# Kernel tuning notes

Hardware: AMD Instinct MI355X
Metric: run time of the kernel (lower is better)

The kernel has to match this reference:

```python
import jax, jax.numpy as jnp
import numpy as np
import math

N_SCALES = 8
WAVELET_LEN = 64
MIN_SCALE, MAX_SCALE = 1.0, 64.0
BATCH, SEQ, FEAT = 16, 4096, 64


def _morlet_init():
    # Faithful to _initialize_mother_wavelets
    t = np.linspace(-4.0, 4.0, WAVELET_LEN, dtype=np.float32)
    w = np.zeros((N_SCALES, WAVELET_LEN), dtype=np.float32)
    for i in range(N_SCALES):
        omega = 2.0 + i * 0.5
        sigma = 1.0 + i * 0.1
        wav = np.exp(-t ** 2 / (2 * sigma ** 2)) * np.cos(omega * t)
        w[i] = wav / np.linalg.norm(wav)
    return jnp.asarray(w)


def setup_inputs() -> dict:
    key = jax.random.key(0)
    k1, _ = jax.random.split(key)
    signal = jax.random.normal(k1, (BATCH, SEQ, FEAT), dtype=jnp.float32)
    mother_wavelets = _morlet_init()
    scale_weights = jnp.ones((N_SCALES,), dtype=jnp.float32)
    return {"signal": signal, "mother_wavelets": mother_wavelets, "scale_weights": scale_weights}


def _scales():
    return np.logspace(math.log10(MIN_SCALE), math.log10(MAX_SCALE), N_SCALES)


def _dilate(wavelet, scale):
    # F.interpolate(mode='linear', align_corners=True) to length int(WAVELET_LEN*scale)
    L_out = int(WAVELET_LEN * scale)
    if L_out > 1:
        pos = jnp.arange(L_out, dtype=jnp.float32) * ((WAVELET_LEN - 1) / (L_out - 1))
    else:
        pos = jnp.zeros((1,), dtype=jnp.float32)
    grid = jnp.arange(WAVELET_LEN, dtype=jnp.float32)
    return jnp.interp(pos, grid, wavelet) / math.sqrt(scale)


def reference(signal, mother_wavelets, scale_weights):
    # signal: (B, S, F) -> coefficients: (B, n_scales, S, F)
    B, S, F = signal.shape
    sig = jnp.swapaxes(signal, 1, 2)  # (B, F, S): batch all FFTs over b,f per scale
    scales = _scales()
    coeffs = []
    for i in range(N_SCALES):
        s = float(scales[i])
        w = _dilate(mother_wavelets[i], s)  # (L_dil,)
        n = S + w.shape[0] - 1
        n_fft = 2 ** int(math.ceil(math.log2(n)))
        Sf = jnp.fft.rfft(sig, n=n_fft, axis=-1)
        Wf = jnp.fft.rfft(w, n=n_fft)
        conv = jnp.fft.irfft(Sf * Wf, n=n_fft, axis=-1)[..., :S]  # (B, F, S)
        coeffs.append(conv)
    C = jnp.stack(coeffs, axis=1)            # (B, n_scales, F, S)
    C = jnp.swapaxes(C, 2, 3)                # (B, n_scales, S, F)
    return C * scale_weights[None, :, None, None]
```

## Files before the change

### kernel.cpp

```cpp
#include <hip/hip_runtime.h>
#include <hip/hip_bf16.h>
#include <math.h>

typedef __attribute__((ext_vector_type(8))) short bf16x8;
typedef __attribute__((ext_vector_type(4))) float f32x4;
typedef __attribute__((ext_vector_type(4))) unsigned int u32x4;
typedef __attribute__((ext_vector_type(2))) unsigned int u32x2;

#define NSC    8
#define SLEN   4096
#define FEAT   64
#define CHUNK_B 8192

#define W4 10176
#define WG_ELEMS 40960
constexpr int L_[NSC]     = {64, 115, 210, 380, 689, 1248, 2261, 4096};
constexpr int LF_[NSC]    = {132, 196, 292, 452, 772, 1316, 2340, 4164};
constexpr int OFF_[NSC]   = {0, 196, 456, 812, 1328, 2164, 3544, 5948};
constexpr int BASES_[NSC] = {132, 392, 748, 1264, 2100, 3480, 5884, 10112};
constexpr int CACT_[NSC]  = {3, 5, 8, 13, 23, 40, 72, 129};

struct WavP { float step[NSC]; float isq[NSC]; };

__global__ void k_build_wav(const float* __restrict__ mw, const float* __restrict__ sw,
                            __hip_bfloat16* __restrict__ wg, WavP wp)
{
  int e = blockIdx.x * 256 + threadIdx.x;
  if (e >= WG_ELEMS) return;
  float val = 0.f;
  if (e < 4 * W4) {
    int q = e / W4;
    int x = e - q * W4;
    int s = 0;
    #pragma unroll
    for (int i = 1; i < NSC; ++i) if (x >= OFF_[i]) s = i;
    int xl = x - OFF_[s] + q;
    int k = LF_[s] - xl;
    if (k >= 0 && k < L_[s]) {
      float pos = (float)k * wp.step[s];
      int ii = (int)pos;
      float r;
      if (ii >= 63) r = mw[s * 64 + 63];
      else {
        float a = mw[s * 64 + ii];
        r = fmaf(pos - (float)ii, mw[s * 64 + ii + 1] - a, a);
      }
      val = r * wp.isq[s] * sw[s];
    }
  }
  wg[e] = __float2bfloat16(val);
}

__global__ __launch_bounds__(256) void k_transpose(const float* __restrict__ sig,
                                                   __hip_bfloat16* __restrict__ sigT2)
{
  __shared__ float t[4096];
  const int tid = threadIdx.x;
  const float* sp = sig + (size_t)blockIdx.x * 4096;
  for (int idx = tid; idx < 4096; idx += 256) {
    int r = idx >> 6, f = idx & 63;
    t[(r << 6) + (f ^ ((r & 7) << 3))] = sp[idx];
  }
  __syncthreads();
  __hip_bfloat16* op = sigT2 + (size_t)blockIdx.x * 4096;
  for (int e = tid; e < 4096; e += 256) {
    int h = e >> 11, n = (e >> 9) & 3, l = (e >> 3) & 63, i = e & 7;
    int f = n * 16 + (l & 15);
    int r = h * 32 + (l >> 4) * 8 + i;
    op[e] = __float2bfloat16(t[(r << 6) + (f ^ ((r & 7) << 3))]);
  }
}

__global__ __launch_bounds__(256, 2) void k_wavelet_mfma(
    const __hip_bfloat16* __restrict__ sigT2,
    const __hip_bfloat16* __restrict__ wavg,
    float* __restrict__ out)
{
  __shared__ __align__(16) short ldsW[WG_ELEMS];

  const int tid = threadIdx.x;
  const int bid = blockIdx.x;
  const int tt  = 63 - (bid >> 4);
  const int b   = bid & 15;
  const int t0  = tt * 64;
  const int tw  = tid >> 6;
  const int fl  = tid & 15;
  const int g   = (tid >> 4) & 3;

  {
    const char* gp = (const char*)wavg;
    char* lp = (char*)ldsW;
    #pragma unroll
    for (int it = 0; it < 20; ++it)
      __builtin_amdgcn_global_load_lds(
        (const __attribute__((address_space(1))) void*)(gp + it * 4096 + tid * 16),
        (__attribute__((address_space(3))) void*)(lp + it * 4096 + (tid >> 6) * 1024),
        16, 0, 0);
  }
  __syncthreads();

  const int q4    = (16 - fl) & 3;
  const int laneA = q4 * W4 + (32 - 16 * tw + 8 * g - fl - q4);

  const int C = tt + 1;
  const char* cb = (const char*)sigT2 + ((size_t)(b * 64 + tt)) * CHUNK_B
                   + (size_t)(tid & 63) * 16;

  f32x4 acc[NSC][4];
  const f32x4 z = {0.f, 0.f, 0.f, 0.f};
  #pragma unroll
  for (int s = 0; s < NSC; ++s)
    #pragma unroll
    for (int n = 0; n < 4; ++n) acc[s][n] = z;

  bf16x8 Ba[8], Bb[8];
  auto loadchunk = [&](int c, bf16x8* B) {
    const char* p = cb - (size_t)c * CHUNK_B;
    #pragma unroll
    for (int hn = 0; hn < 8; ++hn)
      B[hn] = *(const bf16x8*)(p + (hn >> 2) * 4096 + (hn & 3) * 1024);
  };

  auto compute = [&](int c_old, const bf16x8* Bf) {
    const int abase = laneA - 32 * c_old;
    __builtin_amdgcn_s_setprio(1);
    #pragma unroll
    for (int s = NSC - 1; s >= 0; --s) {
      if (c_old <= CACT_[s]) {
        const u32x2* pp = (const u32x2*)(ldsW + abase + BASES_[s]);
        u32x2 w0 = pp[0], w1 = pp[1];
        u32x4 au; au.x = w0.x; au.y = w0.y; au.z = w1.x; au.w = w1.y;
        bf16x8 Af = __builtin_bit_cast(bf16x8, au);
        acc[s][0] = __builtin_amdgcn_mfma_f32_16x16x32_bf16(Af, Bf[0], acc[s][0], 0, 0, 0);
        acc[s][1] = __builtin_amdgcn_mfma_f32_16x16x32_bf16(Af, Bf[1], acc[s][1], 0, 0, 0);
        acc[s][2] = __builtin_amdgcn_mfma_f32_16x16x32_bf16(Af, Bf[2], acc[s][2], 0, 0, 0);
        acc[s][3] = __builtin_amdgcn_mfma_f32_16x16x32_bf16(Af, Bf[3], acc[s][3], 0, 0, 0);
      }
    }
    __builtin_amdgcn_s_setprio(0);
  };

  loadchunk(0, Ba);

  for (int c = 0; c < C; c += 2) {
    loadchunk(c + 1, Bb);
    compute(2 * c,     &Ba[4]);
    compute(2 * c + 1, &Ba[0]);
    loadchunk(c + 2, Ba);
    if (c + 1 < C) {
      compute(2 * c + 2, &Bb[4]);
      compute(2 * c + 3, &Bb[0]);
    }
  }

  const int trow = t0 + tw * 16 + g * 4;
  float* ob = out + (size_t)b * NSC * SLEN * FEAT;
  #pragma unroll
  for (int s = 0; s < NSC; ++s) {
    float* os = ob + (size_t)s * SLEN * FEAT;
    #pragma unroll
    for (int n = 0; n < 4; ++n)
      #pragma unroll
      for (int r = 0; r < 4; ++r)
        os[(size_t)(trow + r) * FEAT + n * 16 + fl] = acc[s][n][r];
  }
}

extern "C" void kernel_launch(void* const* d_in, const int* in_sizes, int n_in,
                              void* d_out, int out_size, void* d_ws, size_t ws_size,
                              hipStream_t stream) {
  const float* sig = (const float*)d_in[0];
  const float* mw  = (const float*)d_in[1];
  const float* sw  = (const float*)d_in[2];
  float*       out = (float*)d_out;

  __hip_bfloat16* wavg  = (__hip_bfloat16*)d_ws;
  __hip_bfloat16* sigT2 = (__hip_bfloat16*)((char*)d_ws + 131072);

  WavP wp;
  const double lg = log10(64.0), st = lg / 7.0;
  for (int i = 0; i < NSC; ++i) {
    double y = (i == 7) ? lg : (double)i * st;
    double s = pow(10.0, y);
    int L = L_[i];
    wp.step[i] = (float)(63.0 / (double)(L - 1));
    wp.isq[i]  = (float)(1.0 / sqrt(s));
  }

  k_build_wav<<<WG_ELEMS / 256, 256, 0, stream>>>(mw, sw, wavg, wp);
  k_transpose<<<1024, 256, 0, stream>>>(sig, sigT2);
  k_wavelet_mfma<<<1024, 256, 0, stream>>>(sigT2, wavg, out);
}
```

Baseline: 83.66 us.

## Replace LDS wavelet staging with precomputed per-lane A-fragment table in global memory

Builds a fully expanded table of bf16 A fragments (one 16-byte vector per lane per scale per quarter-chunk) in global memory, so the main kernel loads A operands directly with vector global loads. This removes the 80KB LDS staging, the block-wide barrier and the unaligned two-part LDS reads. The B-chunk double buffer is also restructured into half-chunk granularity. The cost is about 2MB of table traffic served from L2 instead of LDS, plus extra global load latency inside the MFMA loop.

```diff
diff --git a/kernel.cpp b/kernel.cpp
--- a/kernel.cpp
+++ b/kernel.cpp
@@ -4,51 +4,38 @@
 
 typedef __attribute__((ext_vector_type(8))) short bf16x8;
 typedef __attribute__((ext_vector_type(4))) float f32x4;
-typedef __attribute__((ext_vector_type(4))) unsigned int u32x4;
-typedef __attribute__((ext_vector_type(2))) unsigned int u32x2;
 
 #define NSC    8
 #define SLEN   4096
 #define FEAT   64
 #define CHUNK_B 8192
+#define NQ     258
+#define ATAB_B (NQ * 8 * 1024)
 
-#define W4 10176
-#define WG_ELEMS 40960
-constexpr int L_[NSC]     = {64, 115, 210, 380, 689, 1248, 2261, 4096};
-constexpr int LF_[NSC]    = {132, 196, 292, 452, 772, 1316, 2340, 4164};
-constexpr int OFF_[NSC]   = {0, 196, 456, 812, 1328, 2164, 3544, 5948};
-constexpr int BASES_[NSC] = {132, 392, 748, 1264, 2100, 3480, 5884, 10112};
-constexpr int CACT_[NSC]  = {3, 5, 8, 13, 23, 40, 72, 129};
+constexpr int L_[NSC]    = {64, 115, 210, 380, 689, 1248, 2261, 4096};
+constexpr int CACT_[NSC] = {3, 5, 8, 13, 23, 40, 72, 129};
 
 struct WavP { float step[NSC]; float isq[NSC]; };
 
-__global__ void k_build_wav(const float* __restrict__ mw, const float* __restrict__ sw,
-                            __hip_bfloat16* __restrict__ wg, WavP wp)
+__global__ void k_build_atab(const float* __restrict__ mw, const float* __restrict__ sw,
+                             __hip_bfloat16* __restrict__ at, WavP wp)
 {
   int e = blockIdx.x * 256 + threadIdx.x;
-  if (e >= WG_ELEMS) return;
+  int j = e & 7, l = (e >> 3) & 63, s = (e >> 9) & 7, q = e >> 12;
+  int k = 16 * q - 32 + (l & 15) - 8 * (l >> 4) - j;
   float val = 0.f;
-  if (e < 4 * W4) {
-    int q = e / W4;
-    int x = e - q * W4;
-    int s = 0;
-    #pragma unroll
-    for (int i = 1; i < NSC; ++i) if (x >= OFF_[i]) s = i;
-    int xl = x - OFF_[s] + q;
-    int k = LF_[s] - xl;
-    if (k >= 0 && k < L_[s]) {
-      float pos = (float)k * wp.step[s];
-      int ii = (int)pos;
-      float r;
-      if (ii >= 63) r = mw[s * 64 + 63];
-      else {
-        float a = mw[s * 64 + ii];
-        r = fmaf(pos - (float)ii, mw[s * 64 + ii + 1] - a, a);
-      }
-      val = r * wp.isq[s] * sw[s];
+  if (k >= 0 && k < L_[s]) {
+    float pos = (float)k * wp.step[s];
+    int ii = (int)pos;
+    float r;
+    if (ii >= 63) r = mw[s * 64 + 63];
+    else {
+      float a = mw[s * 64 + ii];
+      r = fmaf(pos - (float)ii, mw[s * 64 + ii + 1] - a, a);
     }
+    val = r * wp.isq[s] * sw[s];
   }
-  wg[e] = __float2bfloat16(val);
+  at[e] = __float2bfloat16(val);
 }
 
 __global__ __launch_bounds__(256) void k_transpose(const float* __restrict__ sig,
@@ -73,38 +60,23 @@
 
 __global__ __launch_bounds__(256, 2) void k_wavelet_mfma(
     const __hip_bfloat16* __restrict__ sigT2,
-    const __hip_bfloat16* __restrict__ wavg,
+    const __hip_bfloat16* __restrict__ atab,
     float* __restrict__ out)
 {
-  __shared__ __align__(16) short ldsW[WG_ELEMS];
-
   const int tid = threadIdx.x;
   const int bid = blockIdx.x;
   const int tt  = 63 - (bid >> 4);
   const int b   = bid & 15;
   const int t0  = tt * 64;
   const int tw  = tid >> 6;
+  const int l   = tid & 63;
   const int fl  = tid & 15;
   const int g   = (tid >> 4) & 3;
 
-  {
-    const char* gp = (const char*)wavg;
-    char* lp = (char*)ldsW;
-    #pragma unroll
-    for (int it = 0; it < 20; ++it)
-      __builtin_amdgcn_global_load_lds(
-        (const __attribute__((address_space(1))) void*)(gp + it * 4096 + tid * 16),
-        (__attribute__((address_space(3))) void*)(lp + it * 4096 + (tid >> 6) * 1024),
-        16, 0, 0);
-  }
-  __syncthreads();
-
-  const int q4    = (16 - fl) & 3;
-  const int laneA = q4 * W4 + (32 - 16 * tw + 8 * g - fl - q4);
-
   const int C = tt + 1;
   const char* cb = (const char*)sigT2 + ((size_t)(b * 64 + tt)) * CHUNK_B
-                   + (size_t)(tid & 63) * 16;
+                   + (size_t)l * 16;
+  const char* aw = (const char*)atab + tw * 8192 + (size_t)l * 16;
 
   f32x4 acc[NSC][4];
   const f32x4 z = {0.f, 0.f, 0.f, 0.f};
@@ -113,44 +85,41 @@
     #pragma unroll
     for (int n = 0; n < 4; ++n) acc[s][n] = z;
 
-  bf16x8 Ba[8], Bb[8];
-  auto loadchunk = [&](int c, bf16x8* B) {
-    const char* p = cb - (size_t)c * CHUNK_B;
+  auto loadB = [&](int c, int h, bf16x8* B) {
+    const char* p = cb - (size_t)c * CHUNK_B + h * 4096;
     #pragma unroll
-    for (int hn = 0; hn < 8; ++hn)
-      B[hn] = *(const bf16x8*)(p + (hn >> 2) * 4096 + (hn & 3) * 1024);
+    for (int n = 0; n < 4; ++n)
+      B[n] = *(const bf16x8*)(p + n * 1024);
   };
 
   auto compute = [&](int c_old, const bf16x8* Bf) {
-    const int abase = laneA - 32 * c_old;
+    const char* pa = aw + (size_t)c_old * 16384;
+    bf16x8 Af[NSC];
+    #pragma unroll
+    for (int s = 0; s < NSC; ++s)
+      if (c_old <= CACT_[s])
+        Af[s] = *(const bf16x8*)(pa + s * 1024);
     __builtin_amdgcn_s_setprio(1);
     #pragma unroll
     for (int s = NSC - 1; s >= 0; --s) {
       if (c_old <= CACT_[s]) {
-        const u32x2* pp = (const u32x2*)(ldsW + abase + BASES_[s]);
-        u32x2 w0 = pp[0], w1 = pp[1];
-        u32x4 au; au.x = w0.x; au.y = w0.y; au.z = w1.x; au.w = w1.y;
-        bf16x8 Af = __builtin_bit_cast(bf16x8, au);
-        acc[s][0] = __builtin_amdgcn_mfma_f32_16x16x32_bf16(Af, Bf[0], acc[s][0], 0, 0, 0);
-        acc[s][1] = __builtin_amdgcn_mfma_f32_16x16x32_bf16(Af, Bf[1], acc[s][1], 0, 0, 0);
-        acc[s][2] = __builtin_amdgcn_mfma_f32_16x16x32_bf16(Af, Bf[2], acc[s][2], 0, 0, 0);
-        acc[s][3] = __builtin_amdgcn_mfma_f32_16x16x32_bf16(Af, Bf[3], acc[s][3], 0, 0, 0);
+        acc[s][0] = __builtin_amdgcn_mfma_f32_16x16x32_bf16(Af[s], Bf[0], acc[s][0], 0, 0, 0);
+        acc[s][1] = __builtin_amdgcn_mfma_f32_16x16x32_bf16(Af[s], Bf[1], acc[s][1], 0, 0, 0);
+        acc[s][2] = __builtin_amdgcn_mfma_f32_16x16x32_bf16(Af[s], Bf[2], acc[s][2], 0, 0, 0);
+        acc[s][3] = __builtin_amdgcn_mfma_f32_16x16x32_bf16(Af[s], Bf[3], acc[s][3], 0, 0, 0);
       }
     }
     __builtin_amdgcn_s_setprio(0);
   };
 
-  loadchunk(0, Ba);
+  bf16x8 B0[4], B1[4];
+  loadB(0, 1, B0);
 
-  for (int c = 0; c < C; c += 2) {
-    loadchunk(c + 1, Bb);
-    compute(2 * c,     &Ba[4]);
-    compute(2 * c + 1, &Ba[0]);
-    loadchunk(c + 2, Ba);
-    if (c + 1 < C) {
-      compute(2 * c + 2, &Bb[4]);
-      compute(2 * c + 3, &Bb[0]);
-    }
+  for (int c = 0; c < C; ++c) {
+    loadB(c, 0, B1);
+    compute(2 * c, B0);
+    loadB(c + 1, 1, B0);
+    compute(2 * c + 1, B1);
   }
 
   const int trow = t0 + tw * 16 + g * 4;
@@ -174,20 +143,19 @@
   const float* sw  = (const float*)d_in[2];
   float*       out = (float*)d_out;
 
-  __hip_bfloat16* wavg  = (__hip_bfloat16*)d_ws;
-  __hip_bfloat16* sigT2 = (__hip_bfloat16*)((char*)d_ws + 131072);
+  __hip_bfloat16* atab  = (__hip_bfloat16*)d_ws;
+  __hip_bfloat16* sigT2 = (__hip_bfloat16*)((char*)d_ws + 0x220000);
 
   WavP wp;
   const double lg = log10(64.0), st = lg / 7.0;
   for (int i = 0; i < NSC; ++i) {
     double y = (i == 7) ? lg : (double)i * st;
     double s = pow(10.0, y);
-    int L = L_[i];
-    wp.step[i] = (float)(63.0 / (double)(L - 1));
+    wp.step[i] = (float)(63.0 / (double)(L_[i] - 1));
     wp.isq[i]  = (float)(1.0 / sqrt(s));
   }
 
-  k_build_wav<<<WG_ELEMS / 256, 256, 0, stream>>>(mw, sw, wavg, wp);
+  k_build_atab<<<NQ * 8 * 512 / 256, 256, 0, stream>>>(mw, sw, atab, wp);
   k_transpose<<<1024, 256, 0, stream>>>(sig, sigT2);
-  k_wavelet_mfma<<<1024, 256, 0, stream>>>(sigT2, wavg, out);
+  k_wavelet_mfma<<<1024, 256, 0, stream>>>(sigT2, atab, out);
 }
```

Measured after the change: 98.80 us. 1.18x slower.
